# Optimization experiments

Measured on AMD Instinct MI355X. Metric: run time of the kernel, lower is better.

Reference implementation:

```python
import jax, jax.numpy as jnp
import numpy as np
from jax import lax

ATT_ITERS = 3


def setup_inputs() -> dict:
    key = jax.random.key(0)
    ks = jax.random.split(key, 18)
    B, N, DI, DO, R = 32, 64, 256, 256, 256
    def lin(kw, kb, fan_in, fan_out):
        W = jax.random.normal(kw, (fan_in, fan_out), jnp.float32) / np.float32(np.sqrt(fan_in))
        b = jax.random.normal(kb, (fan_out,), jnp.float32) * 0.01
        return W, b
    W_self, b_self = lin(ks[0], ks[1], DI, R)
    W_srep, b_srep = lin(ks[2], ks[3], DO, R)
    W_skey, b_skey = lin(ks[4], ks[5], DO, R)
    W_forget, b_forget = lin(ks[6], ks[7], 4 * R, R)
    W_hid, b_hid = lin(ks[8], ks[9], 4 * R, R)
    W_query, b_query = lin(ks[10], ks[11], 3 * R, R)
    W_out, b_out = lin(ks[12], ks[13], 3 * R, DO)
    nodes = jax.random.normal(ks[14], (B, N, DI), jnp.float32)
    adj = jnp.ones((B, N, N), jnp.float32)  # src_conn; all-ones keeps denominators nonzero
    return {
        'nodes': nodes, 'adj': adj,
        'W_self': W_self, 'b_self': b_self,
        'W_srep': W_srep, 'b_srep': b_srep,
        'W_skey': W_skey, 'b_skey': b_skey,
        'W_forget': W_forget, 'b_forget': b_forget,
        'W_hid': W_hid, 'b_hid': b_hid,
        'W_query': W_query, 'b_query': b_query,
        'W_out': W_out, 'b_out': b_out,
    }


def reference(nodes, adj, W_self, b_self, W_srep, b_srep, W_skey, b_skey,
              W_forget, b_forget, W_hid, b_hid, W_query, b_query, W_out, b_out):
    B, N, _ = nodes.shape
    R = W_self.shape[1]
    DO = W_out.shape[1]
    dt = nodes.dtype

    node_id_rep = nodes @ W_self + b_self  # [B, N, R]
    out0 = jnp.zeros((B, N, DO), dt)

    def step(out_nodes, xs):
        rep_i, mask_i, idx = xs  # [B,R], [B,N], scalar node index
        src_rep = out_nodes @ W_srep + b_srep    # [B, N, R]
        src_keys = out_nodes @ W_skey + b_skey   # [B, N, R]
        hidden = jnp.zeros((B, R), dt)
        query = jnp.zeros((B, R), dt)
        for _ in range(ATT_ITERS):
            att = jnp.einsum('bk,bik->bi', query, src_keys)           # [B, N]
            att = jnp.exp(att - jnp.max(att, axis=1, keepdims=True))
            att = att * mask_i
            att = att / jnp.sum(att, axis=1, keepdims=True)
            query_res = jnp.einsum('bi,bir->br', att, src_rep)        # [B, R]
            f_in = jnp.concatenate((query_res, hidden, rep_i, query), axis=1)
            forget = jax.nn.sigmoid(f_in @ W_forget + b_forget)
            h_in = jnp.concatenate((query_res, forget * hidden, rep_i, query), axis=1)
            hidden = forget * hidden + (1 - forget) * jnp.tanh(h_in @ W_hid + b_hid)
            q_in = jnp.concatenate((hidden, rep_i, query), axis=1)
            query = q_in @ W_query + b_query
        o_in = jnp.concatenate((hidden, rep_i, query), axis=1)
        out_i = o_in @ W_out + b_out                                  # [B, DO]
        out_nodes = out_nodes.at[:, idx].set(out_i)
        return out_nodes, None

    xs = (jnp.transpose(node_id_rep, (1, 0, 2)),  # [N, B, R]
          jnp.transpose(adj, (2, 0, 1)),          # [N, B, N]: mask of sources into node i
          jnp.arange(N))
    out_nodes, _ = lax.scan(step, out0, xs)
    return (out_nodes, adj)
```

## Files before the change

### kernel.cpp

```cpp
#include <hip/hip_runtime.h>
#include <hip/hip_bf16.h>

typedef unsigned int u32;
typedef unsigned short u16;
typedef u32 u32x4 __attribute__((ext_vector_type(4)));
typedef _Float16 h16x2 __attribute__((ext_vector_type(2)));


struct G4 { const float* Bm[4]; const float* bias[4]; float* C[4]; };

__global__ __launch_bounds__(256) void gemm16(const float* __restrict__ A, G4 g) {
  __shared__ float At[16 * 256];
  const int sub = blockIdx.y;
  const float* __restrict__ Bm = g.Bm[sub];
  const float* __restrict__ bias = g.bias[sub];
  float* __restrict__ C = g.C[sub];
  const int r0 = blockIdx.x * 16;
  const int t = threadIdx.x;
#pragma unroll
  for (int j = 0; j < 16; ++j) At[j * 256 + t] = A[(r0 + j) * 256 + t];
  __syncthreads();
  float acc[16];
#pragma unroll
  for (int j = 0; j < 16; ++j) acc[j] = 0.f;
  for (int k = 0; k < 256; ++k) {
    const float bv = Bm[k * 256 + t];
#pragma unroll
    for (int j = 0; j < 16; ++j) acc[j] = fmaf(At[j * 256 + k], bv, acc[j]);
  }
  const float bs = bias[t];
#pragma unroll
  for (int j = 0; j < 16; ++j) C[(r0 + j) * 256 + t] = acc[j] + bs;
}

__global__ __launch_bounds__(256) void gemmD(const float* __restrict__ A,
                                             const float* __restrict__ B,
                                             const float* __restrict__ D,
                                             float* __restrict__ C) {
  __shared__ float At[16 * 256];
  const int r0 = blockIdx.x * 16;
  const int t = threadIdx.x;
#pragma unroll
  for (int j = 0; j < 16; ++j) At[j * 256 + t] = A[(r0 + j) * 256 + t];
  __syncthreads();
  float acc[16];
#pragma unroll
  for (int j = 0; j < 16; ++j) acc[j] = 0.f;
  for (int k = 0; k < 256; ++k) {
    const float bv = B[k * 256 + t];
#pragma unroll
    for (int j = 0; j < 16; ++j) acc[j] = fmaf(At[j * 256 + k], bv, acc[j]);
  }
#pragma unroll
  for (int j = 0; j < 16; ++j) {
    const float dv = D ? D[(r0 + j) * 256 + t] : 0.f;
    C[(r0 + j) * 256 + t] = acc[j] + dv;
  }
}

struct C12 { const float* src[12]; };

__device__ __forceinline__ u16 f16b(float x) {
  union { _Float16 h; u16 u; } c; c.h = (_Float16)x; return c.u;
}
__device__ __forceinline__ u32 pk2f(float a, float b) {
  return (u32)f16b(a) | ((u32)f16b(b) << 16);
}
__device__ __forceinline__ float f16f(u16 x) {
  union { u16 u; _Float16 h; } c; c.u = x; return (float)c.h;
}
__device__ __forceinline__ h16x2 ash2(u32 x) {
  union { u32 u; h16x2 h; } c; c.u = x; return c.h;
}

#if __has_builtin(__builtin_amdgcn_fdot2)
#define FDOT2(A, W, X) A = __builtin_amdgcn_fdot2(ash2(W), ash2(X), A, false)
#else
#define FDOT2(A, W, X) \
  asm("v_dot2_f32_f16 %0, %1, %2, %0" : "+v"(A) : "v"(W), "v"(X))
#endif

__global__ __launch_bounds__(256) void cvt_panels(C12 c, u16* __restrict__ dst) {
  const int z = blockIdx.y;
  const float* __restrict__ in = c.src[z];
  const int e = blockIdx.x * 256 + threadIdx.x;
  const int j = e & 7, l = (e >> 3) & 63, r = (e >> 9) & 7;
  const int cc = (e >> 12) & 1, w8 = e >> 13;
  const int col = w8 * 32 + (l & 31);
  const int k = (2 * (l >> 5) + cc) * 64 + r * 8 + j;
  dst[z * 65536 + e] = f16b(in[k * 256 + col]);
}

#define PID_F1 0

#define OFF_SREPT 0
#define OFF_SKEY  9216
#define OFF_ATTW  17664
#define OFF_XQR   17920
#define OFF_XFH   18048
#define OFF_XO    18176
#define OFF_H2    18304
#define OFF_Q2    18560
#define LDS_U32   18816

#define BAR() asm volatile("s_waitcnt lgkmcnt(0)\n\ts_barrier" ::: "memory")
#define SB()  __builtin_amdgcn_sched_barrier(0)

__device__ __forceinline__ float sgm(float x) { return 1.f / (1.f + __expf(-x)); }
__device__ __forceinline__ float tnh(float x) { return 1.f - 2.f / (__expf(2.f * x) + 1.f); }

__device__ __forceinline__ int pid_of(int idx) {
  const unsigned long long P0 = 0x5321067453210630ull;
  const unsigned long long P1 = 0x00000000000BA984ull;
  const unsigned long long v = (idx < 16) ? (P0 >> (idx * 4))
                                          : (P1 >> ((idx - 16) * 4));
  return (int)(v & 15);
}

#define DE(x, d) ((u32)(x) | ((u32)(d) << 16))
__device__ const u32 ITBL[21] = {
  DE(OFF_XQR,       0x80),
  DE(OFF_XQR,       0xC1),
  DE(OFF_H2,        0xA4),
  DE(OFF_XQR,       0x80),
  DE(OFF_H2,        0x00),
  DE(OFF_Q2,        0x00),
  DE(OFF_XQR,       0xC0),
  DE(OFF_Q2,        0x42),
  DE(OFF_XFH,       0x40),
  DE(OFF_Q2,        0x8B),
  DE(OFF_H2 + 128,  0x2C),
  DE(OFF_XQR,       0x80),
  DE(OFF_H2 + 128,  0x00),
  DE(OFF_Q2 + 128,  0x00),
  DE(OFF_XQR,       0xC0),
  DE(OFF_Q2 + 128,  0x4A),
  DE(OFF_XFH,       0x43),
  DE(OFF_H2,        0x80),
  DE(OFF_Q2 + 128,  0x05),
  DE(OFF_XO,        0x86),
  DE(OFF_XO,        0x87)};

#define ISSQ(BUF, P, C) {                                                     \
    const u32* gp_ = pan_lane + (((P) << 15) + ((C) << 11));                  \
    _Pragma("unroll")                                                         \
    for (int r_ = 0; r_ < 8; ++r_) BUF[r_] = *(const u32x4*)(gp_ + (r_ << 8)); \
    SB(); }

__device__ __forceinline__ float cq(const u32x4 (&buf)[8], const u32* xq) {
  float a = 0.f;
#pragma unroll
  for (int r = 0; r < 8; ++r) {
    const u32x4 wv = buf[r];
    const u32x4 xv = *(const u32x4*)(xq + (r << 2));
    FDOT2(a, wv[0], xv[0]); FDOT2(a, wv[1], xv[1]);
    FDOT2(a, wv[2], xv[2]); FDOT2(a, wv[3], xv[3]);
  }
  return a;
}

__device__ __forceinline__ void qres_phase(u32* lds, int w8, int col) {
  float qr = 0.f;
  const u32* sp = lds + OFF_SREPT + col * 36;
  const u32* ap = lds + OFF_ATTW + (w8 << 5);
#pragma unroll
  for (int nq = 0; nq < 8; ++nq) {
    const u32x4 sv = *(const u32x4*)(sp + (nq << 2));
    const u32x4 av = *(const u32x4*)(ap + (nq << 2));
    FDOT2(qr, sv[0], av[0]); FDOT2(qr, sv[1], av[1]);
    FDOT2(qr, sv[2], av[2]); FDOT2(qr, sv[3], av[3]);
  }
  ((u16*)(lds + OFF_XQR))[col] = f16b(qr);
}

__device__ __forceinline__ void logits_phase(u32* lds, int w8, int l,
                                             float mk, int cp) {
  float la = 0.f;
  const u32* kp = lds + OFF_SKEY + l * 132;
  const u32* qp = lds + OFF_Q2 + cp * 128;
#pragma unroll
  for (int kq = 0; kq < 32; ++kq) {
    const u32x4 kv = *(const u32x4*)(kp + (((u32)(kq << 2)) ^ ((l & 7) << 2)));
    const u32x4 qv = *(const u32x4*)(qp + (kq << 2));
    FDOT2(la, kv[0], qv[0]); FDOT2(la, kv[1], qv[1]);
    FDOT2(la, kv[2], qv[2]); FDOT2(la, kv[3], qv[3]);
  }
  float mx = la;
#pragma unroll
  for (int o = 1; o < 64; o <<= 1) mx = fmaxf(mx, __shfl_xor(mx, o, 64));
  const float e = __expf(la - mx) * mk;
  float sm = e;
#pragma unroll
  for (int o = 1; o < 64; o <<= 1) sm += __shfl_xor(sm, o, 64);
  ((u16*)(lds + OFF_ATTW))[(w8 << 6) + l] = f16b(e / sm);
}

__global__ __launch_bounds__(512) void dagsage_main(
    const float* __restrict__ adj,
    const float* __restrict__ b_srep, const float* __restrict__ b_skey,
    const float* __restrict__ pf, const float* __restrict__ ph,
    const float* __restrict__ pq, const float* __restrict__ poO,
    const u16* __restrict__ panels,
    float* __restrict__ outp) {
  __shared__ u32 lds[LDS_U32];
  const int t = threadIdx.x;
  const int w8 = t >> 6, l = t & 63;
  const int g = l >> 5;
  const int col = (w8 << 5) + (l & 31);
  const int xq0 = g << 6;
  const int b = blockIdx.x;

  {
    const float bs0 = b_srep[col];
    for (int j = g * 16; j < g * 16 + 16; ++j)
      lds[OFF_SREPT + col * 36 + j] = pk2f(bs0, bs0);
    const int n = t >> 3, kk0 = (t & 7) * 16;
    for (int j = 0; j < 16; ++j) {
      const int kk = kk0 + j;
      lds[OFF_SKEY + n * 132 + (((u32)kk) ^ ((n & 7) << 2))] =
          pk2f(b_skey[2 * kk], b_skey[2 * kk + 1]);
    }
  }
  __syncthreads();

  const float bsv = b_srep[col];
  const float bkv = b_skey[col];
  const u32* pan_lane = (const u32*)panels + (w8 << 12) + (l << 2);

  u32x4 bufA[8], bufB[8];
  ISSQ(bufA, PID_F1, 0);

#pragma unroll 1
  for (int i = 0; i < 64; ++i) {
    const int ro = (b * 64 + i) * 256 + col;
    const float pfv = pf[ro], phv = ph[ro], pqv = pq[ro], pov = poO[ro];
    const float mk = adj[(b * 64 + l) * 64 + i];

    {
      float sm = mk;
#pragma unroll
      for (int o = 1; o < 64; o <<= 1) sm += __shfl_xor(sm, o, 64);
      ((u16*)(lds + OFF_ATTW))[(w8 << 6) + l] = f16b(mk / sm);
    }
    qres_phase(lds, w8, col);
    BAR();

    float a0 = 0.f, a1 = 0.f, frv = 0.f, fhv = 0.f;

#pragma unroll 1
    for (int it = 0; it < 21; ++it) {
      const u32 cur = ITBL[it];
      const u32 d = cur >> 16;
      const u32* xq = lds + (cur & 0xFFFF) + xq0;
      const int pc = pid_of(it);
      const int pn = pid_of(it + 1);

      float acc;
      ISSQ(bufB, pc, 1); acc  = cq(bufA, xq);      SB();
      ISSQ(bufA, pn, 0); acc += cq(bufB, xq + 32); SB();

      if (d & 0x80) { if (d & 0x40) a1 = acc;  else a0 = acc; }
      else          { if (d & 0x40) a1 += acc; else a0 += acc; }

      const int tl = d & 7;
      if (tl) {
        const int p = (d >> 3) & 1;
        const float A0 = a0 + __shfl_xor(a0, 32, 64);
        const float A1 = a1 + __shfl_xor(a1, 32, 64);
        switch (tl) {
          case 1: {
            frv = sgm(A0 + pfv);
            ((u16*)(lds + OFF_H2))[col] = f16b((1.f - frv) * tnh(A1 + phv));
          } break;
          case 2: {
            frv = sgm(A0 + pfv);
            fhv = frv * f16f(((const u16*)(lds + OFF_H2))[p * 256 + col]);
            ((u16*)(lds + OFF_XFH))[col] = f16b(fhv);
          } break;
          case 3: {
            ((u16*)(lds + OFF_H2))[p * 256 + col] =
                f16b(fhv + (1.f - frv) * tnh(A1 + phv));
          } break;
          case 4: {
            ((u16*)(lds + OFF_Q2))[p * 256 + col] = f16b(A0 + pqv);
          } break;
          case 5: {
            const float ov = A0 + pov;
            if (l < 32) outp[ro] = ov;
            ((u16*)(lds + OFF_XO))[col] = f16b(ov);
          } break;
          case 6: {
            ((u16*)(lds + OFF_SREPT))[col * 72 + i] = f16b(A0 + bsv);
          } break;
          case 7: {
            ((u16*)(lds + OFF_SKEY))[i * 264 + (((u32)col) ^ ((i & 7) << 3))] =
                f16b(A0 + bkv);
          } break;
          default: break;
        }
        if (tl < 6) BAR();
        if ((tl == 4) && (d & 0x20)) {
          logits_phase(lds, w8, l, mk, p);
          qres_phase(lds, w8, col);
          BAR();
        }
      }
    }
  }
}

extern "C" void kernel_launch(void* const* d_in, const int* in_sizes, int n_in,
                              void* d_out, int out_size, void* d_ws, size_t ws_size,
                              hipStream_t stream) {
  const float* nodes    = (const float*)d_in[0];
  const float* adj      = (const float*)d_in[1];
  const float* W_self   = (const float*)d_in[2];
  const float* b_self   = (const float*)d_in[3];
  const float* W_srep   = (const float*)d_in[4];
  const float* b_srep   = (const float*)d_in[5];
  const float* W_skey   = (const float*)d_in[6];
  const float* b_skey   = (const float*)d_in[7];
  const float* W_forget = (const float*)d_in[8];
  const float* b_forget = (const float*)d_in[9];
  const float* W_hid    = (const float*)d_in[10];
  const float* b_hid    = (const float*)d_in[11];
  const float* W_query  = (const float*)d_in[12];
  const float* b_query  = (const float*)d_in[13];
  const float* W_out    = (const float*)d_in[14];
  const float* b_out    = (const float*)d_in[15];
  float* out = (float*)d_out;

  float* rep = (float*)d_ws;
  float* pf  = rep + 524288;
  float* ph  = pf + 524288;
  float* pq  = ph + 524288;
  float* po  = pq + 524288;
  u16* panels = (u16*)(po + 524288);
  float* tmpA = pf;
  float* tmpB = pf + 65536;

  const float* Q1 = W_query;
  const float* O3 = W_out + 512 * 256;

  hipMemcpyAsync(out + 524288, adj, 131072 * sizeof(float),
                 hipMemcpyDeviceToDevice, stream);

  gemmD<<<16, 256, 0, stream>>>(Q1, O3, W_out, tmpA);
  gemmD<<<16, 256, 0, stream>>>(W_query + 512 * 256, O3, nullptr, tmpB);

  C12 ca;
  ca.src[0]  = W_forget;
  ca.src[1]  = W_forget + 256 * 256;
  ca.src[2]  = W_forget + 768 * 256;
  ca.src[3]  = W_hid;
  ca.src[4]  = W_hid + 256 * 256;
  ca.src[5]  = W_hid + 768 * 256;
  ca.src[6]  = W_query;
  ca.src[7]  = W_query + 512 * 256;
  ca.src[8]  = tmpA;
  ca.src[9]  = tmpB;
  ca.src[10] = W_srep;
  ca.src[11] = W_skey;
  cvt_panels<<<dim3(256, 12), 256, 0, stream>>>(ca, panels);

  G4 g1;
  for (int j = 0; j < 4; ++j) { g1.Bm[j] = W_self; g1.bias[j] = b_self; g1.C[j] = rep; }
  gemm16<<<dim3(128, 1), 256, 0, stream>>>(nodes, g1);

  G4 g2;
  g2.Bm[0] = W_forget + 512 * 256; g2.bias[0] = b_forget; g2.C[0] = pf;
  g2.Bm[1] = W_hid + 512 * 256;    g2.bias[1] = b_hid;    g2.C[1] = ph;
  g2.Bm[2] = W_query + 256 * 256;  g2.bias[2] = b_query;  g2.C[2] = pq;
  g2.Bm[3] = W_out + 256 * 256;    g2.bias[3] = b_out;    g2.C[3] = po;
  gemm16<<<dim3(128, 4), 256, 0, stream>>>(rep, g2);

  gemmD<<<128, 256, 0, stream>>>(pq, O3, po, po);

  dagsage_main<<<32, 512, 0, stream>>>(adj, b_srep, b_skey,
                                       pf, ph, pq, po, panels, out);
}
```

Before: 2.058 ms.

## Triple-buffer weight panel prefetch and switch LDS swizzle to padded strides

```diff
diff --git a/kernel.cpp b/kernel.cpp
--- a/kernel.cpp
+++ b/kernel.cpp
@@ -94,14 +94,14 @@
 #define PID_F1 0
 
 #define OFF_SREPT 0
-#define OFF_SKEY  9216
-#define OFF_ATTW  17664
-#define OFF_XQR   17920
-#define OFF_XFH   18048
-#define OFF_XO    18176
-#define OFF_H2    18304
-#define OFF_Q2    18560
-#define LDS_U32   18816
+#define OFF_SKEY  9472
+#define OFF_ATTW  17984
+#define OFF_XQR   18240
+#define OFF_XFH   18368
+#define OFF_XO    18496
+#define OFF_H2    18624
+#define OFF_Q2    18880
+#define LDS_U32   19136
 
 #define BAR() asm volatile("s_waitcnt lgkmcnt(0)\n\ts_barrier" ::: "memory")
 #define SB()  __builtin_amdgcn_sched_barrier(0)
@@ -161,7 +161,7 @@
 
 __device__ __forceinline__ void qres_phase(u32* lds, int w8, int col) {
   float qr = 0.f;
-  const u32* sp = lds + OFF_SREPT + col * 36;
+  const u32* sp = lds + OFF_SREPT + col * 37;
   const u32* ap = lds + OFF_ATTW + (w8 << 5);
 #pragma unroll
   for (int nq = 0; nq < 8; ++nq) {
@@ -176,11 +176,11 @@
 __device__ __forceinline__ void logits_phase(u32* lds, int w8, int l,
                                              float mk, int cp) {
   float la = 0.f;
-  const u32* kp = lds + OFF_SKEY + l * 132;
+  const u32* kp = lds + OFF_SKEY + l * 133;
   const u32* qp = lds + OFF_Q2 + cp * 128;
 #pragma unroll
   for (int kq = 0; kq < 32; ++kq) {
-    const u32x4 kv = *(const u32x4*)(kp + (((u32)(kq << 2)) ^ ((l & 7) << 2)));
+    const u32x4 kv = *(const u32x4*)(kp + (kq << 2));
     const u32x4 qv = *(const u32x4*)(qp + (kq << 2));
     FDOT2(la, kv[0], qv[0]); FDOT2(la, kv[1], qv[1]);
     FDOT2(la, kv[2], qv[2]); FDOT2(la, kv[3], qv[3]);
@@ -213,11 +213,11 @@
   {
     const float bs0 = b_srep[col];
     for (int j = g * 16; j < g * 16 + 16; ++j)
-      lds[OFF_SREPT + col * 36 + j] = pk2f(bs0, bs0);
+      lds[OFF_SREPT + col * 37 + j] = pk2f(bs0, bs0);
     const int n = t >> 3, kk0 = (t & 7) * 16;
     for (int j = 0; j < 16; ++j) {
       const int kk = kk0 + j;
-      lds[OFF_SKEY + n * 132 + (((u32)kk) ^ ((n & 7) << 2))] =
+      lds[OFF_SKEY + n * 133 + kk] =
           pk2f(b_skey[2 * kk], b_skey[2 * kk + 1]);
     }
   }
@@ -227,8 +227,64 @@
   const float bkv = b_skey[col];
   const u32* pan_lane = (const u32*)panels + (w8 << 12) + (l << 2);
 
-  u32x4 bufA[8], bufB[8];
+  u32x4 bufA[8], bufB[8], bufC[8];
   ISSQ(bufA, PID_F1, 0);
+  ISSQ(bufB, PID_F1, 1);
+
+#define ITEM(B0, B1, B2, IT) {                                                \
+    const u32 cur = ITBL[IT];                                                 \
+    const u32 d = cur >> 16;                                                  \
+    const u32* xq = lds + (cur & 0xFFFF) + xq0;                               \
+    const int pn = pid_of((IT) + 1);                                          \
+    ISSQ(B2, pn, 0);                                                          \
+    float acc = cq(B0, xq); SB();                                             \
+    ISSQ(B0, pn, 1);                                                          \
+    acc += cq(B1, xq + 32); SB();                                             \
+    if (d & 0x80) { if (d & 0x40) a1 = acc;  else a0 = acc; }                 \
+    else          { if (d & 0x40) a1 += acc; else a0 += acc; }                 \
+    const int tl = d & 7;                                                     \
+    if (tl) {                                                                 \
+      const int p = (d >> 3) & 1;                                             \
+      const float A0 = a0 + __shfl_xor(a0, 32, 64);                           \
+      const float A1 = a1 + __shfl_xor(a1, 32, 64);                           \
+      switch (tl) {                                                           \
+        case 1: {                                                    \
+          frv = sgm(A0 + pfv);                                                \
+          ((u16*)(lds + OFF_H2))[col] = f16b((1.f - frv) * tnh(A1 + phv));    \
+        } break;                                                              \
+        case 2: {                                                      \
+          frv = sgm(A0 + pfv);                                                \
+          fhv = frv * f16f(((const u16*)(lds + OFF_H2))[p * 256 + col]);      \
+          ((u16*)(lds + OFF_XFH))[col] = f16b(fhv);                           \
+        } break;                                                              \
+        case 3: {                                                      \
+          ((u16*)(lds + OFF_H2))[p * 256 + col] =                             \
+              f16b(fhv + (1.f - frv) * tnh(A1 + phv));                        \
+        } break;                                                              \
+        case 4: {                                                      \
+          ((u16*)(lds + OFF_Q2))[p * 256 + col] = f16b(A0 + pqv);             \
+        } break;                                                              \
+        case 5: {                             \
+          const float ov = A0 + pov;                                          \
+          if (l < 32) outp[ro] = ov;                                          \
+          ((u16*)(lds + OFF_XO))[col] = f16b(ov);                             \
+        } break;                                                              \
+        case 6: {         \
+          ((u16*)(lds + OFF_SREPT))[col * 74 + i] = f16b(A0 + bsv);           \
+        } break;                                                              \
+        case 7: {         \
+          ((u16*)(lds + OFF_SKEY))[i * 266 + col] = f16b(A0 + bkv);           \
+        } break;                                                              \
+        default: break;                                                       \
+      }                                                                       \
+      if (tl < 6) BAR();                                                      \
+      if ((tl == 4) && (d & 0x20)) {        \
+        logits_phase(lds, w8, l, mk, p);                                      \
+        qres_phase(lds, w8, col);                                             \
+        BAR();                                                                \
+      }                                                                       \
+    }                                                                         \
+  }
 
 #pragma unroll 1
   for (int i = 0; i < 64; ++i) {
@@ -248,63 +304,10 @@
     float a0 = 0.f, a1 = 0.f, frv = 0.f, fhv = 0.f;
 
 #pragma unroll 1
-    for (int it = 0; it < 21; ++it) {
-      const u32 cur = ITBL[it];
-      const u32 d = cur >> 16;
-      const u32* xq = lds + (cur & 0xFFFF) + xq0;
-      const int pc = pid_of(it);
-      const int pn = pid_of(it + 1);
-
-      float acc;
-      ISSQ(bufB, pc, 1); acc  = cq(bufA, xq);      SB();
-      ISSQ(bufA, pn, 0); acc += cq(bufB, xq + 32); SB();
-
-      if (d & 0x80) { if (d & 0x40) a1 = acc;  else a0 = acc; }
-      else          { if (d & 0x40) a1 += acc; else a0 += acc; }
-
-      const int tl = d & 7;
-      if (tl) {
-        const int p = (d >> 3) & 1;
-        const float A0 = a0 + __shfl_xor(a0, 32, 64);
-        const float A1 = a1 + __shfl_xor(a1, 32, 64);
-        switch (tl) {
-          case 1: {
-            frv = sgm(A0 + pfv);
-            ((u16*)(lds + OFF_H2))[col] = f16b((1.f - frv) * tnh(A1 + phv));
-          } break;
-          case 2: {
-            frv = sgm(A0 + pfv);
-            fhv = frv * f16f(((const u16*)(lds + OFF_H2))[p * 256 + col]);
-            ((u16*)(lds + OFF_XFH))[col] = f16b(fhv);
-          } break;
-          case 3: {
-            ((u16*)(lds + OFF_H2))[p * 256 + col] =
-                f16b(fhv + (1.f - frv) * tnh(A1 + phv));
-          } break;
-          case 4: {
-            ((u16*)(lds + OFF_Q2))[p * 256 + col] = f16b(A0 + pqv);
-          } break;
-          case 5: {
-            const float ov = A0 + pov;
-            if (l < 32) outp[ro] = ov;
-            ((u16*)(lds + OFF_XO))[col] = f16b(ov);
-          } break;
-          case 6: {
-            ((u16*)(lds + OFF_SREPT))[col * 72 + i] = f16b(A0 + bsv);
-          } break;
-          case 7: {
-            ((u16*)(lds + OFF_SKEY))[i * 264 + (((u32)col) ^ ((i & 7) << 3))] =
-                f16b(A0 + bkv);
-          } break;
-          default: break;
-        }
-        if (tl < 6) BAR();
-        if ((tl == 4) && (d & 0x20)) {
-          logits_phase(lds, w8, l, mk, p);
-          qres_phase(lds, w8, col);
-          BAR();
-        }
-      }
+    for (int itg = 0; itg < 21; itg += 3) {
+      ITEM(bufA, bufB, bufC, itg);
+      ITEM(bufC, bufA, bufB, itg + 1);
+      ITEM(bufB, bufC, bufA, itg + 2);
     }
   }
 }
```

New measurement: 2.951 ms. +43.3%, slower.
